# Kernel optimization log

Hardware: AMD Instinct MI355X
Metric: run time of the kernel (lower is better)

The kernel has to match this reference:

```python
import jax, jax.numpy as jnp
import numpy as np

T, B, C, H, W = 128, 16, 4, 84, 84
NUM_ACTIONS, FEAT, HID = 18, 512, 256


def _conv(x, w, b, stride):
    # x: (N,C,H,W), w: (O,I,kh,kw)
    y = jax.lax.conv_general_dilated(
        x, w, window_strides=(stride, stride), padding='VALID',
        dimension_numbers=('NCHW', 'OIHW', 'NCHW'))
    return y + b[None, :, None, None]


def setup_inputs() -> dict:
    key = jax.random.key(0)
    ks = jax.random.split(key, 24)
    s = 0.05
    inp = {
        'obs_seq': jax.random.uniform(ks[0], (T, B, C, H, W), jnp.float32) * 255.0,
        'actions_seq': jax.random.randint(ks[1], (T, B), 0, NUM_ACTIONS),
        'episode_starts_seq': jax.random.randint(ks[2], (T, B), 0, 2).astype(jnp.float32),
        'h0': jnp.zeros((1, B, HID), jnp.float32),
        'c0': jnp.zeros((1, B, HID), jnp.float32),
        # NatureCNN params
        'conv1_w': jax.random.normal(ks[3], (32, C, 8, 8)) * s,
        'conv1_b': jnp.zeros((32,)),
        'conv2_w': jax.random.normal(ks[4], (64, 32, 4, 4)) * s,
        'conv2_b': jnp.zeros((64,)),
        'conv3_w': jax.random.normal(ks[5], (64, 64, 3, 3)) * s,
        'conv3_b': jnp.zeros((64,)),
        'fc_w': jax.random.normal(ks[6], (FEAT, 64 * 7 * 7)) * s,
        'fc_b': jnp.zeros((FEAT,)),
        # LSTM params (torch gate order i,f,g,o)
        'w_ih': jax.random.normal(ks[7], (4 * HID, FEAT)) * s,
        'w_hh': jax.random.normal(ks[8], (4 * HID, HID)) * s,
        'b_ih': jnp.zeros((4 * HID,)),
        'b_hh': jnp.zeros((4 * HID,)),
        # heads
        'actor_w': jax.random.normal(ks[9], (NUM_ACTIONS, HID)) * 0.01,
        'actor_b': jnp.zeros((NUM_ACTIONS,)),
        'critic_w': jax.random.normal(ks[10], (1, HID)) * s,
        'critic_b': jnp.zeros((1,)),
        'aux_w': jax.random.normal(ks[11], (1, FEAT)) * s,
        'aux_b': jnp.zeros((1,)),
    }
    return inp


def reference(obs_seq, actions_seq, episode_starts_seq, h0, c0,
              conv1_w, conv1_b, conv2_w, conv2_b, conv3_w, conv3_b,
              fc_w, fc_b, w_ih, w_hh, b_ih, b_hh,
              actor_w, actor_b, critic_w, critic_b, aux_w, aux_b):
    t, b = actions_seq.shape
    x = obs_seq.reshape(t * b, *obs_seq.shape[2:]) / 255.0
    x = jax.nn.relu(_conv(x, conv1_w, conv1_b, 4))   # (TB,32,20,20)
    x = jax.nn.relu(_conv(x, conv2_w, conv2_b, 2))   # (TB,64,9,9)
    x = jax.nn.relu(_conv(x, conv3_w, conv3_b, 1))   # (TB,64,7,7)
    feat = jax.nn.relu(x.reshape(t * b, -1) @ fc_w.T + fc_b)  # (TB,FEAT)

    aux_logits = (feat @ aux_w.T + aux_b).squeeze(-1).reshape(t, b)
    feat_seq = feat.reshape(t, b, -1)

    def step(carry, inp):
        h, c = carry
        x_t, s_t = inp
        keep = (1.0 - s_t)[:, None]
        h = h * keep
        c = c * keep
        gates = x_t @ w_ih.T + b_ih + h @ w_hh.T + b_hh  # (B,4H)
        i, f, g, o = jnp.split(gates, 4, axis=-1)
        c = jax.nn.sigmoid(f) * c + jax.nn.sigmoid(i) * jnp.tanh(g)
        h = jax.nn.sigmoid(o) * jnp.tanh(c)
        return (h, c), h

    _, out = jax.lax.scan(step, (h0[0], c0[0]), (feat_seq, episode_starts_seq))  # (T,B,HID)

    logits = out @ actor_w.T + actor_b
    logp = jax.nn.log_softmax(logits, axis=-1)
    log_probs = jnp.take_along_axis(logp, actions_seq[..., None], axis=-1).squeeze(-1)
    entropy = -jnp.sum(jnp.exp(logp) * logp, axis=-1)
    values = (out @ critic_w.T + critic_b).squeeze(-1)
    return log_probs, entropy, values, aux_logits
```

## Files before the change

kernel.cpp:

```cpp
#include <hip/hip_runtime.h>
#include <hip/hip_bf16.h>
#include <cstddef>

typedef __attribute__((ext_vector_type(8))) short bf16x8;
typedef __attribute__((ext_vector_type(8))) unsigned short u16x8;
typedef __attribute__((ext_vector_type(4))) float f32x4;

static constexpr size_t OFF_X1B   = 0;
static constexpr size_t OFF_X2B   = 52428800;
static constexpr size_t OFF_X3B   = 73662464;
static constexpr size_t OFF_FEATB = 86507520;
static constexpr size_t OFF_W2B   = 88604672;
static constexpr size_t OFF_W3B   = 88670208;
static constexpr size_t OFF_FCWB  = 88743936;
static constexpr size_t OFF_WIHB  = 91955200;
static constexpr size_t OFF_GX    = 97198080;
static constexpr size_t OFF_HSEQ  = 105586688;
static constexpr size_t OFF_W1B   = 108732416;
static constexpr size_t OFF_WHHB  = 108748800;
static constexpr size_t OFF_ORDB  = 109273088;
static constexpr size_t OFF_ORDT0 = 109281280;
static constexpr size_t OFF_ORDLEN= 109289472;
static constexpr size_t OFF_NSEG  = 109297664;
static constexpr size_t OFF_FCPART= 109305856;

__device__ __forceinline__ float sigmoidf_(float x) {
  return 1.0f / (1.0f + __expf(-x));
}
__device__ __forceinline__ float tanhf_(float x) {
  return 1.0f - 2.0f / (__expf(2.0f * x) + 1.0f);
}
__device__ __forceinline__ unsigned short f2bfu(float x) {
  union { __hip_bfloat16 b; unsigned short u; } cv;
  cv.b = __float2bfloat16(x);
  return cv.u;
}

__global__ __launch_bounds__(256) void prep_kernel(
    const float* __restrict__ c1w, const float* __restrict__ c2w,
    const float* __restrict__ c3w, const float* __restrict__ fcw,
    const float* __restrict__ wih, const float* __restrict__ whh,
    __hip_bfloat16* __restrict__ w1b,
    __hip_bfloat16* __restrict__ w2b, __hip_bfloat16* __restrict__ w3b,
    __hip_bfloat16* __restrict__ fcwb, __hip_bfloat16* __restrict__ wihb,
    __hip_bfloat16* __restrict__ whhb) {
  int i = blockIdx.x * 256 + threadIdx.x;
  if (i < 32768) {
    int o = i >> 9, k = i & 511;
    int pos = k >> 5, ci = k & 31;
    int ky = pos >> 2, kx = pos & 3;
    w2b[i] = __float2bfloat16(c2w[o * 512 + ci * 16 + ky * 4 + kx]);
  } else if (i < 69632) {
    int j = i - 32768;
    int o = j / 576, k = j - o * 576;
    int pos = k >> 6, ci = k & 63;
    int ky = pos / 3, kx = pos - ky * 3;
    w3b[j] = __float2bfloat16(c3w[o * 576 + ci * 9 + ky * 3 + kx]);
  } else if (i < 1675264) {
    int j = i - 69632;
    int o = j / 3136, k = j - o * 3136;
    int sp = k >> 6, ci = k & 63;
    fcwb[j] = __float2bfloat16(fcw[o * 3136 + ci * 49 + sp]);
  } else if (i < 2199552) {
    int j = i - 1675264;
    wihb[j] = __float2bfloat16(wih[j]);
  } else if (i < 2461696) {
    int j = i - 2199552;
    whhb[j] = __float2bfloat16(whh[j]);
  } else if (i < 2469888) {
    int j = i - 2461696;
    int oc = j >> 8, k = j & 255;
    int ky = k >> 5, rem = k & 31;
    int ci = rem >> 3, kx = rem & 7;
    w1b[j] = __float2bfloat16(c1w[oc * 256 + ci * 64 + ky * 8 + kx] * (1.0f / 255.0f));
  }
}

__global__ __launch_bounds__(256) void plan_kernel(
    const float* __restrict__ starts, int* __restrict__ ord_b,
    int* __restrict__ ord_t0, int* __restrict__ ord_len,
    int* __restrict__ nseg_out) {
  __shared__ float s_starts[2048];
  __shared__ int s_t0[2048];
  __shared__ int s_len[2048];
  __shared__ int cnt[16];
  __shared__ int hist[132];
  __shared__ int off[132];
  const int tid = threadIdx.x;
  {
    float4* d = (float4*)s_starts;
    const float4* s = (const float4*)starts;
#pragma unroll
    for (int i = 0; i < 2; ++i) d[tid + i * 256] = s[tid + i * 256];
  }
  if (tid < 132) hist[tid] = 0;
  __syncthreads();
  if (tid < 16) {
    int b = tid, c = 0;
    for (int t = 0; t < 128; ++t) {
      float s = s_starts[t * 16 + b];
      if (t == 0 || s != 0.0f) {
        if (c > 0) s_len[b * 128 + c - 1] = t - s_t0[b * 128 + c - 1];
        s_t0[b * 128 + c] = t;
        ++c;
      }
    }
    s_len[b * 128 + c - 1] = 128 - s_t0[b * 128 + c - 1];
    cnt[b] = c;
  }
  __syncthreads();
  for (int idx = tid; idx < 2048; idx += 256) {
    int b = idx >> 7, i = idx & 127;
    if (i < cnt[b]) atomicAdd(&hist[s_len[idx]], 1);
  }
  __syncthreads();
  if (tid == 0) {
    int running = 0;
    for (int L = 128; L >= 1; --L) { off[L] = running; running += hist[L]; }
    *nseg_out = running;
  }
  __syncthreads();
  for (int idx = tid; idx < 2048; idx += 256) {
    int b = idx >> 7, i = idx & 127;
    if (i < cnt[b]) {
      int len = s_len[idx];
      int pos = atomicAdd(&off[len], 1);
      ord_b[pos] = b;
      ord_t0[pos] = s_t0[idx];
      ord_len[pos] = len;
    }
  }
}

__global__ __launch_bounds__(256, 2) void conv1_img(
    const float* __restrict__ obs, const __hip_bfloat16* __restrict__ w1b,
    const float* __restrict__ bias1, __hip_bfloat16* __restrict__ x1b) {
  constexpr int LDW = 264;
  __shared__ __align__(16) __hip_bfloat16 img[28224];
  __shared__ __align__(16) __hip_bfloat16 Ws[32 * LDW];
  const int tid = threadIdx.x;
  const int wv = tid >> 6, l = tid & 63;
  const int lane16 = l & 15, quad = l >> 4;
  const int n = blockIdx.x;

  for (int i = tid; i < 1024; i += 256) {
    const int r = i >> 5, c = (i & 31) * 8;
    *(uint4*)&Ws[r * LDW + c] = *(const uint4*)&w1b[r * 256 + c];
  }
  const float4* obs4 = (const float4*)(obs + (size_t)n * 28224);
  for (int j = tid; j < 7056; j += 256) {
    const float4 v = obs4[j];
    const int xq = j % 21;
    const int yc = j / 21;
    const int c = yc / 84, y = yc - c * 84;
    ushort4 w;
    w.x = f2bfu(v.x); w.y = f2bfu(v.y); w.z = f2bfu(v.z); w.w = f2bfu(v.w);
    *(ushort4*)&img[(y * 4 + c) * 84 + xq * 4] = w;
  }
  __syncthreads();

  const float bb0 = bias1[lane16];
  const float bb1 = bias1[16 + lane16];
  const __hip_bfloat16* wr0 = &Ws[lane16 * LDW];
  const __hip_bfloat16* wr1 = &Ws[(16 + lane16) * LDW];

  for (int f = wv; f < 25; f += 4) {
    const int sp = f * 16 + lane16;
    const int oy = sp / 20, ox = sp - oy * 20;
    const int ab = ((oy * 4) * 4 + quad) * 84 + ox * 4;
    f32x4 acc0 = {}, acc1 = {};
#pragma unroll
    for (int s = 0; s < 8; ++s) {
      const int ib = ab + s * 4 * 84;
      const ushort4 lo = *(const ushort4*)&img[ib];
      const ushort4 hi = *(const ushort4*)&img[ib + 4];
      bf16x8 a;
      a[0] = (short)lo.x; a[1] = (short)lo.y; a[2] = (short)lo.z; a[3] = (short)lo.w;
      a[4] = (short)hi.x; a[5] = (short)hi.y; a[6] = (short)hi.z; a[7] = (short)hi.w;
      const bf16x8 b0 = *(const bf16x8*)&wr0[s * 32 + quad * 8];
      const bf16x8 b1v = *(const bf16x8*)&wr1[s * 32 + quad * 8];
      acc0 = __builtin_amdgcn_mfma_f32_16x16x32_bf16(a, b0, acc0, 0, 0, 0);
      acc1 = __builtin_amdgcn_mfma_f32_16x16x32_bf16(a, b1v, acc1, 0, 0, 0);
    }
#pragma unroll
    for (int r = 0; r < 4; ++r) {
      const size_t row = (size_t)n * 400 + f * 16 + quad * 4 + r;
      x1b[row * 32 + lane16] = __float2bfloat16(fmaxf(acc0[r] + bb0, 0.f));
      x1b[row * 32 + 16 + lane16] = __float2bfloat16(fmaxf(acc1[r] + bb1, 0.f));
    }
  }
}

template<int KK, int LDW, int MODE>
__global__ __launch_bounds__(256, 2) void conv_rs(
    const __hip_bfloat16* __restrict__ A, const __hip_bfloat16* __restrict__ Wb,
    const float* __restrict__ bias, __hip_bfloat16* __restrict__ Cb) {
  __shared__ __align__(16) __hip_bfloat16 Ws[64 * LDW];
  const int tid = threadIdx.x;
  const int wv = tid >> 6, l = tid & 63;
  const int lane16 = l & 15, quad = l >> 4;
  constexpr int CPR = KK / 8;
  constexpr int CH = 64 * CPR;
  for (int i = tid; i < CH; i += 256) {
    const int r = i / CPR;
    const int c = (i - r * CPR) * 8;
    *(uint4*)&Ws[r * LDW + c] = *(const uint4*)&Wb[r * KK + c];
  }
  const int m0 = blockIdx.x * 256 + wv * 64;
  const __hip_bfloat16* abase[4];
#pragma unroll
  for (int mf = 0; mf < 4; ++mf) {
    const int m = m0 + mf * 16 + lane16;
    if (MODE == 1) {
      const int n = m / 81, sp = m - n * 81;
      const int oy = sp / 9, ox = sp - oy * 9;
      abase[mf] = A + ((n * 20 + oy * 2) * 20 + ox * 2) * 32 + quad * 8;
    } else {
      const int n = m / 49, sp = m - n * 49;
      const int oy = sp / 7, ox = sp - oy * 7;
      abase[mf] = A + ((n * 9 + oy) * 9 + ox) * 64 + quad * 8;
    }
  }
  f32x4 acc[4][4] = {};
  __syncthreads();
  constexpr int KS = KK / 32;
#pragma unroll
  for (int s = 0; s < KS; ++s) {
    int koff;
    if (MODE == 1) {
      koff = ((s >> 2) * 20 + (s & 3)) * 32;
    } else {
      const int pos = s >> 1;
      koff = ((pos / 3) * 9 + (pos % 3)) * 64 + (s & 1) * 32;
    }
    bf16x8 bfr[4];
#pragma unroll
    for (int nf = 0; nf < 4; ++nf)
      bfr[nf] = *(const bf16x8*)&Ws[(nf * 16 + lane16) * LDW + s * 32 + quad * 8];
#pragma unroll
    for (int mf = 0; mf < 4; ++mf) {
      const bf16x8 a = *(const bf16x8*)(abase[mf] + koff);
#pragma unroll
      for (int nf = 0; nf < 4; ++nf)
        acc[mf][nf] = __builtin_amdgcn_mfma_f32_16x16x32_bf16(a, bfr[nf], acc[mf][nf], 0, 0, 0);
    }
  }
#pragma unroll
  for (int nf = 0; nf < 4; ++nf) {
    const int col = nf * 16 + lane16;
    const float bb = bias[col];
#pragma unroll
    for (int mf = 0; mf < 4; ++mf)
#pragma unroll
      for (int r = 0; r < 4; ++r) {
        const int row = m0 + mf * 16 + quad * 4 + r;
        Cb[(size_t)row * 64 + col] =
            __float2bfloat16(fmaxf(acc[mf][nf][r] + bb, 0.f));
      }
  }
}

template<int BM, int MODE>
__global__ __launch_bounds__(256) void gemm_mfma(
    const __hip_bfloat16* __restrict__ Abase,
    const __hip_bfloat16* __restrict__ Wb,
    const float* __restrict__ bias1, const float* __restrict__ bias2,
    float* __restrict__ Cf, __hip_bfloat16* __restrict__ Cb,
    const int M, const int N, const int K, const int relu,
    float* __restrict__ Cpart) {
  constexpr int LDK = 40;
  __shared__ __align__(16) __hip_bfloat16 As[BM * LDK];
  __shared__ __align__(16) __hip_bfloat16 Ws[64 * LDK];
  const int tid = threadIdx.x;
  const int m0 = blockIdx.y * BM;
  const int n0 = blockIdx.x * 64;
  const int l = tid & 63;
  const int wv = tid >> 6;
  const int lane16 = l & 15;
  const int quad = l >> 4;
  constexpr int NF = (BM == 128) ? 4 : 2;
  const int m_base = (BM == 128) ? wv * 32 : (wv & 1) * 32;
  const int n_base = (BM == 128) ? 0 : (wv >> 1) * 32;
  constexpr int NCA = (BM == 128) ? 2 : 1;

  f32x4 acc[2][NF] = {};

  const __hip_bfloat16* arow[NCA];
  int acp[NCA];
#pragma unroll
  for (int c = 0; c < NCA; ++c) {
    const int id = tid + c * 256;
    const int row = id >> 2, cpos = id & 3;
    const int m = m0 + row;
    acp[c] = cpos;
    arow[c] = Abase + (size_t)m * K + cpos * 8;
  }
  const int wrow = tid >> 2, wcp = tid & 3;
  const __hip_bfloat16* wsrc = Wb + (size_t)(n0 + wrow) * K + wcp * 8;

  int s0 = 0, s1 = K >> 5;
  if (Cpart) {
    const int total = K >> 5;
    const int zz = blockIdx.z;
    const int q = total >> 2, rr = total & 3;
    s0 = zz * q + (zz < rr ? zz : rr);
    s1 = s0 + q + (zz < rr ? 1 : 0);
  }
  for (int s = s0; s < s1; ++s) {
    uint4 av[NCA];
#pragma unroll
    for (int c = 0; c < NCA; ++c) {
      av[c] = *(const uint4*)(arow[c] + s * 32);
    }
    const uint4 wval = *(const uint4*)(wsrc + s * 32);
    __syncthreads();
#pragma unroll
    for (int c = 0; c < NCA; ++c) {
      const int row = (tid + c * 256) >> 2;
      *(uint4*)&As[row * LDK + acp[c] * 8] = av[c];
    }
    *(uint4*)&Ws[wrow * LDK + wcp * 8] = wval;
    __syncthreads();
    const bf16x8 a0 = *(const bf16x8*)&As[(m_base + lane16) * LDK + quad * 8];
    const bf16x8 a1 = *(const bf16x8*)&As[(m_base + 16 + lane16) * LDK + quad * 8];
#pragma unroll
    for (int nf = 0; nf < NF; ++nf) {
      const bf16x8 b = *(const bf16x8*)&Ws[(n_base + nf * 16 + lane16) * LDK + quad * 8];
      acc[0][nf] = __builtin_amdgcn_mfma_f32_16x16x32_bf16(a0, b, acc[0][nf], 0, 0, 0);
      acc[1][nf] = __builtin_amdgcn_mfma_f32_16x16x32_bf16(a1, b, acc[1][nf], 0, 0, 0);
    }
  }
  if (Cpart) {
    float* dst = Cpart + (size_t)blockIdx.z * M * N;
#pragma unroll
    for (int nf = 0; nf < NF; ++nf) {
      const int col = n0 + n_base + nf * 16 + lane16;
#pragma unroll
      for (int mf = 0; mf < 2; ++mf) {
#pragma unroll
        for (int r = 0; r < 4; ++r) {
          const int row = m0 + m_base + mf * 16 + quad * 4 + r;
          dst[(size_t)row * N + col] = acc[mf][nf][r];
        }
      }
    }
    return;
  }
#pragma unroll
  for (int nf = 0; nf < NF; ++nf) {
    const int col = n0 + n_base + nf * 16 + lane16;
    float bb = bias1[col];
    if (bias2) bb += bias2[col];
#pragma unroll
    for (int mf = 0; mf < 2; ++mf) {
#pragma unroll
      for (int r = 0; r < 4; ++r) {
        const int row = m0 + m_base + mf * 16 + quad * 4 + r;
        float v = acc[mf][nf][r] + bb;
        if (relu) v = fmaxf(v, 0.f);
        if (Cf) Cf[(size_t)row * N + col] = v;
        if (Cb) Cb[(size_t)row * N + col] = __float2bfloat16(v);
      }
    }
  }
}

__global__ __launch_bounds__(256) void fc_reduce(
    const float* __restrict__ part, const float* __restrict__ fcb,
    const float* __restrict__ aux_w, const float* __restrict__ aux_b,
    __hip_bfloat16* __restrict__ featb, float* __restrict__ outp) {
  const int row = blockIdx.x;
  const int tid = threadIdx.x;
  __shared__ float red[256];
  float auxacc = 0.f;
#pragma unroll
  for (int h = 0; h < 2; ++h) {
    const int c = tid + h * 256;
    const size_t base = (size_t)row * 512 + c;
    float v = part[base] + part[1048576 + base] + part[2097152 + base] +
              part[3145728 + base];
    v += fcb[c];
    v = fmaxf(v, 0.f);
    featb[base] = __float2bfloat16(v);
    auxacc += v * aux_w[c];
  }
  red[tid] = auxacc;
  __syncthreads();
  for (int s = 128; s > 0; s >>= 1) {
    if (tid < s) red[tid] += red[tid + s];
    __syncthreads();
  }
  if (tid == 0) outp[6144 + row] = red[0] + aux_b[0];
}

__global__ __launch_bounds__(1024, 4) void lstm_mfma(
    const float* __restrict__ gx, const __hip_bfloat16* __restrict__ whhb,
    const float* __restrict__ starts, const float* __restrict__ h0,
    const float* __restrict__ c0, const int* __restrict__ ord_b,
    const int* __restrict__ ord_t0, const int* __restrict__ ord_len,
    const int* __restrict__ nseg_p, float* __restrict__ hseq) {
  constexpr int LDH = 264;
  constexpr int PS  = 1028;
  __shared__ __align__(16) __hip_bfloat16 h_lds[16 * LDH];
  __shared__ __align__(16) float pre[16 * PS];
  __shared__ int sg_b[16], sg_t0[16], sg_len[16];
  const int g = blockIdx.x;
  const int nseg = *nseg_p;
  if (g * 16 >= nseg) return;
  const int tid = threadIdx.x;
  const int wv = tid >> 6;
  const int l = tid & 63;
  const int lane16 = l & 15, quad = l >> 4;
  if (tid < 16) {
    const int s = g * 16 + tid;
    sg_b[tid] = (s < nseg) ? ord_b[s] : 0;
    sg_t0[tid] = (s < nseg) ? ord_t0[s] : 0;
    sg_len[tid] = (s < nseg) ? ord_len[s] : 0;
  }
  __syncthreads();
  bf16x8 bfrag[2][8];
#pragma unroll
  for (int nt = 0; nt < 2; ++nt)
#pragma unroll
    for (int ks = 0; ks < 8; ++ks)
      bfrag[nt][ks] = *(const bf16x8*)&whhb[
          (size_t)(wv * 64 + nt * 16 + lane16) * 256 + ks * 32 + quad * 8];
  const __hip_bfloat16* bs2 = &whhb[(size_t)(wv * 64 + 32 + lane16) * 256 + quad * 8];
  const __hip_bfloat16* bs3 = &whhb[(size_t)(wv * 64 + 48 + lane16) * 256 + quad * 8];

  const int m_own = wv;
  const int u = l * 4;
  const int b_own = sg_b[m_own];
  const int t0_own = sg_t0[m_own];
  const int len_own = sg_len[m_own];
  float4 c_reg = make_float4(0.f, 0.f, 0.f, 0.f);
  {
    float4 hv = make_float4(0.f, 0.f, 0.f, 0.f);
    if (len_own > 0 && t0_own == 0) {
      const float keep = 1.0f - starts[b_own];
      const float4 h4 = *(const float4*)&h0[b_own * 256 + u];
      const float4 c4 = *(const float4*)&c0[b_own * 256 + u];
      hv = make_float4(h4.x * keep, h4.y * keep, h4.z * keep, h4.w * keep);
      c_reg = make_float4(c4.x * keep, c4.y * keep, c4.z * keep, c4.w * keep);
    }
    __hip_bfloat16* hd = &h_lds[m_own * LDH + u];
    hd[0] = __float2bfloat16(hv.x); hd[1] = __float2bfloat16(hv.y);
    hd[2] = __float2bfloat16(hv.z); hd[3] = __float2bfloat16(hv.w);
  }
  const int maxlen = sg_len[0];
  for (int tt = 0; tt < maxlen; ++tt) {
    __syncthreads();
    f32x4 acc[4] = {};
#pragma unroll
    for (int ks = 0; ks < 8; ++ks) {
      const bf16x8 b2 = *(const bf16x8*)(bs2 + ks * 32);
      const bf16x8 b3 = *(const bf16x8*)(bs3 + ks * 32);
      const bf16x8 a = *(const bf16x8*)&h_lds[lane16 * LDH + ks * 32 + quad * 8];
      acc[0] = __builtin_amdgcn_mfma_f32_16x16x32_bf16(a, bfrag[0][ks], acc[0], 0, 0, 0);
      acc[1] = __builtin_amdgcn_mfma_f32_16x16x32_bf16(a, bfrag[1][ks], acc[1], 0, 0, 0);
      acc[2] = __builtin_amdgcn_mfma_f32_16x16x32_bf16(a, b2, acc[2], 0, 0, 0);
      acc[3] = __builtin_amdgcn_mfma_f32_16x16x32_bf16(a, b3, acc[3], 0, 0, 0);
    }
#pragma unroll
    for (int nt = 0; nt < 4; ++nt)
#pragma unroll
      for (int r = 0; r < 4; ++r)
        pre[(quad * 4 + r) * PS + wv * 64 + nt * 16 + lane16] = acc[nt][r];
    __syncthreads();
    if (tt < len_own) {
      const int t = t0_own + tt;
      const size_t gbase = (size_t)(t * 16 + b_own) * 1024 + u;
      const float4 g0 = *(const float4*)&gx[gbase];
      const float4 g1 = *(const float4*)&gx[gbase + 256];
      const float4 g2 = *(const float4*)&gx[gbase + 512];
      const float4 g3 = *(const float4*)&gx[gbase + 768];
      const float4 p0 = *(const float4*)&pre[m_own * PS + u];
      const float4 p1 = *(const float4*)&pre[m_own * PS + u + 256];
      const float4 p2 = *(const float4*)&pre[m_own * PS + u + 512];
      const float4 p3 = *(const float4*)&pre[m_own * PS + u + 768];
      const float i0 = sigmoidf_(p0.x + g0.x), i1 = sigmoidf_(p0.y + g0.y),
                  i2 = sigmoidf_(p0.z + g0.z), i3 = sigmoidf_(p0.w + g0.w);
      const float f0 = sigmoidf_(p1.x + g1.x), f1 = sigmoidf_(p1.y + g1.y),
                  f2 = sigmoidf_(p1.z + g1.z), f3 = sigmoidf_(p1.w + g1.w);
      const float q0 = tanhf_(p2.x + g2.x), q1 = tanhf_(p2.y + g2.y),
                  q2 = tanhf_(p2.z + g2.z), q3 = tanhf_(p2.w + g2.w);
      const float o0 = sigmoidf_(p3.x + g3.x), o1 = sigmoidf_(p3.y + g3.y),
                  o2 = sigmoidf_(p3.z + g3.z), o3 = sigmoidf_(p3.w + g3.w);
      c_reg.x = fmaf(f0, c_reg.x, i0 * q0);
      c_reg.y = fmaf(f1, c_reg.y, i1 * q1);
      c_reg.z = fmaf(f2, c_reg.z, i2 * q2);
      c_reg.w = fmaf(f3, c_reg.w, i3 * q3);
      const float4 h4 = make_float4(o0 * tanhf_(c_reg.x), o1 * tanhf_(c_reg.y),
                                    o2 * tanhf_(c_reg.z), o3 * tanhf_(c_reg.w));
      __hip_bfloat16* hd = &h_lds[m_own * LDH + u];
      hd[0] = __float2bfloat16(h4.x); hd[1] = __float2bfloat16(h4.y);
      hd[2] = __float2bfloat16(h4.z); hd[3] = __float2bfloat16(h4.w);
      *(float4*)&hseq[(size_t)(t * 16 + b_own) * 256 + u] = h4;
    }
  }
}

__global__ __launch_bounds__(256) void heads_kernel(
    const float* __restrict__ hseq, const int* __restrict__ actions,
    const float* __restrict__ actor_w, const float* __restrict__ actor_b,
    const float* __restrict__ critic_w, const float* __restrict__ critic_b,
    float* __restrict__ outp) {
  const int tid = threadIdx.x;
  const int wv = tid >> 6, l = tid & 63;
  const int tb = blockIdx.x * 4 + wv;
  const float4 h4 = *(const float4*)&hseq[(size_t)tb * 256 + l * 4];
  float part[19];
#pragma unroll
  for (int o = 0; o < 18; ++o) {
    const float4 w = *(const float4*)&actor_w[o * 256 + l * 4];
    part[o] = h4.x * w.x + h4.y * w.y + h4.z * w.z + h4.w * w.w;
  }
  {
    const float4 w = *(const float4*)&critic_w[l * 4];
    part[18] = h4.x * w.x + h4.y * w.y + h4.z * w.z + h4.w * w.w;
  }
#pragma unroll
  for (int off = 32; off > 0; off >>= 1) {
#pragma unroll
    for (int o = 0; o < 19; ++o) part[o] += __shfl_xor(part[o], off);
  }
  float lg[18];
  float m = -1e30f;
#pragma unroll
  for (int o = 0; o < 18; ++o) {
    lg[o] = part[o] + actor_b[o];
    m = fmaxf(m, lg[o]);
  }
  float se = 0.f;
#pragma unroll
  for (int o = 0; o < 18; ++o) se += __expf(lg[o] - m);
  const float lse = __logf(se);
  float ent = 0.f;
#pragma unroll
  for (int o = 0; o < 18; ++o) {
    const float lp = lg[o] - m - lse;
    ent -= __expf(lp) * lp;
  }
  if (l == 0) {
    const int a = actions[tb];
    outp[tb] = lg[a] - m - lse;
    outp[2048 + tb] = ent;
    outp[4096 + tb] = part[18] + critic_b[0];
  }
}

extern "C" void kernel_launch(void* const* d_in, const int* in_sizes, int n_in,
                              void* d_out, int out_size, void* d_ws, size_t ws_size,
                              hipStream_t stream) {
  const float* obs     = (const float*)d_in[0];
  const int*   actions = (const int*)d_in[1];
  const float* starts  = (const float*)d_in[2];
  const float* h0      = (const float*)d_in[3];
  const float* c0      = (const float*)d_in[4];
  const float* c1w     = (const float*)d_in[5];
  const float* c1b     = (const float*)d_in[6];
  const float* c2w     = (const float*)d_in[7];
  const float* c2b     = (const float*)d_in[8];
  const float* c3w     = (const float*)d_in[9];
  const float* c3b     = (const float*)d_in[10];
  const float* fcw     = (const float*)d_in[11];
  const float* fcb     = (const float*)d_in[12];
  const float* wih     = (const float*)d_in[13];
  const float* whh     = (const float*)d_in[14];
  const float* bih     = (const float*)d_in[15];
  const float* bhh     = (const float*)d_in[16];
  const float* aw      = (const float*)d_in[17];
  const float* ab      = (const float*)d_in[18];
  const float* cw      = (const float*)d_in[19];
  const float* cb      = (const float*)d_in[20];
  const float* auxw    = (const float*)d_in[21];
  const float* auxb    = (const float*)d_in[22];

  char* ws = (char*)d_ws;
  __hip_bfloat16* x1b   = (__hip_bfloat16*)(ws + OFF_X1B);
  __hip_bfloat16* x2b   = (__hip_bfloat16*)(ws + OFF_X2B);
  __hip_bfloat16* x3b   = (__hip_bfloat16*)(ws + OFF_X3B);
  __hip_bfloat16* featb = (__hip_bfloat16*)(ws + OFF_FEATB);
  __hip_bfloat16* w2b   = (__hip_bfloat16*)(ws + OFF_W2B);
  __hip_bfloat16* w3b   = (__hip_bfloat16*)(ws + OFF_W3B);
  __hip_bfloat16* fcwb  = (__hip_bfloat16*)(ws + OFF_FCWB);
  __hip_bfloat16* wihb  = (__hip_bfloat16*)(ws + OFF_WIHB);
  __hip_bfloat16* w1b   = (__hip_bfloat16*)(ws + OFF_W1B);
  __hip_bfloat16* whhb  = (__hip_bfloat16*)(ws + OFF_WHHB);
  float* gx   = (float*)(ws + OFF_GX);
  float* hseq = (float*)(ws + OFF_HSEQ);
  int* ord_b   = (int*)(ws + OFF_ORDB);
  int* ord_t0  = (int*)(ws + OFF_ORDT0);
  int* ord_len = (int*)(ws + OFF_ORDLEN);
  int* nseg    = (int*)(ws + OFF_NSEG);
  float* fcpart= (float*)(ws + OFF_FCPART);
  float* outp = (float*)d_out;

  prep_kernel<<<9648, 256, 0, stream>>>(c1w, c2w, c3w, fcw, wih, whh,
                                        w1b, w2b, w3b, fcwb, wihb, whhb);
  plan_kernel<<<1, 256, 0, stream>>>(starts, ord_b, ord_t0, ord_len, nseg);
  conv1_img<<<2048, 256, 0, stream>>>(obs, w1b, c1b, x1b);
  conv_rs<512, 520, 1><<<648, 256, 0, stream>>>(x1b, w2b, c2b, x2b);
  conv_rs<576, 584, 2><<<392, 256, 0, stream>>>(x2b, w3b, c3b, x3b);
  gemm_mfma<64, 0><<<dim3(8, 32, 4), 256, 0, stream>>>(
      x3b, fcwb, fcb, nullptr, nullptr, nullptr, 2048, 512, 3136, 0, fcpart);
  fc_reduce<<<2048, 256, 0, stream>>>(fcpart, fcb, auxw, auxb, featb, outp);
  gemm_mfma<64, 0><<<dim3(16, 32), 256, 0, stream>>>(
      featb, wihb, bih, bhh, gx, nullptr, 2048, 1024, 512, 0, nullptr);
  lstm_mfma<<<128, 1024, 0, stream>>>(gx, whhb, starts, h0, c0,
                                      ord_b, ord_t0, ord_len, nseg, hseq);
  heads_kernel<<<512, 256, 0, stream>>>(hseq, actions, aw, ab, cw, cb, outp);
}
```

Measured before the change: 658.3 us.

## Restructure conv stages with direct global-to-LDS loads and per-image blocks

```diff
diff --git a/kernel.cpp b/kernel.cpp
--- a/kernel.cpp
+++ b/kernel.cpp
@@ -3,26 +3,25 @@
 #include <cstddef>
 
 typedef __attribute__((ext_vector_type(8))) short bf16x8;
-typedef __attribute__((ext_vector_type(8))) unsigned short u16x8;
 typedef __attribute__((ext_vector_type(4))) float f32x4;
 
 static constexpr size_t OFF_X1B   = 0;
-static constexpr size_t OFF_X2B   = 52428800;
-static constexpr size_t OFF_X3B   = 73662464;
-static constexpr size_t OFF_FEATB = 86507520;
-static constexpr size_t OFF_W2B   = 88604672;
-static constexpr size_t OFF_W3B   = 88670208;
-static constexpr size_t OFF_FCWB  = 88743936;
-static constexpr size_t OFF_WIHB  = 91955200;
-static constexpr size_t OFF_GX    = 97198080;
-static constexpr size_t OFF_HSEQ  = 105586688;
-static constexpr size_t OFF_W1B   = 108732416;
-static constexpr size_t OFF_WHHB  = 108748800;
-static constexpr size_t OFF_ORDB  = 109273088;
-static constexpr size_t OFF_ORDT0 = 109281280;
-static constexpr size_t OFF_ORDLEN= 109289472;
-static constexpr size_t OFF_NSEG  = 109297664;
-static constexpr size_t OFF_FCPART= 109305856;
+static constexpr size_t OFF_X2B   = 65536000;
+static constexpr size_t OFF_X3B   = 89423872;
+static constexpr size_t OFF_FEATB = 102268928;
+static constexpr size_t OFF_W2B   = 104366080;
+static constexpr size_t OFF_W3B   = 104431616;
+static constexpr size_t OFF_FCWB  = 104505344;
+static constexpr size_t OFF_WIHB  = 107716608;
+static constexpr size_t OFF_GX    = 108765184;
+static constexpr size_t OFF_HSEQ  = 117153792;
+static constexpr size_t OFF_W1B   = 119250944;
+static constexpr size_t OFF_WHHB  = 119267328;
+static constexpr size_t OFF_ORDB  = 119791616;
+static constexpr size_t OFF_ORDT0 = 119799808;
+static constexpr size_t OFF_ORDLEN= 119808000;
+static constexpr size_t OFF_NSEG  = 119816192;
+static constexpr size_t OFF_FCPART= 119824384;
 
 __device__ __forceinline__ float sigmoidf_(float x) {
   return 1.0f / (1.0f + __expf(-x));
@@ -30,10 +29,15 @@
 __device__ __forceinline__ float tanhf_(float x) {
   return 1.0f - 2.0f / (__expf(2.0f * x) + 1.0f);
 }
-__device__ __forceinline__ unsigned short f2bfu(float x) {
-  union { __hip_bfloat16 b; unsigned short u; } cv;
+__device__ __forceinline__ short f2bfs(float x) {
+  union { __hip_bfloat16 b; short s; } cv;
   cv.b = __float2bfloat16(x);
-  return cv.u;
+  return cv.s;
+}
+__device__ __forceinline__ void dma16(const void* g, void* l) {
+  __builtin_amdgcn_global_load_lds(
+      (const __attribute__((address_space(1))) unsigned int*)g,
+      (__attribute__((address_space(3))) unsigned int*)l, 16, 0, 0);
 }
 
 __global__ __launch_bounds__(256) void prep_kernel(
@@ -132,131 +136,174 @@
   }
 }
 
-__global__ __launch_bounds__(256, 2) void conv1_img(
+__global__ __launch_bounds__(256, 2) void conv1_dma(
     const float* __restrict__ obs, const __hip_bfloat16* __restrict__ w1b,
     const float* __restrict__ bias1, __hip_bfloat16* __restrict__ x1b) {
   constexpr int LDW = 264;
-  __shared__ __align__(16) __hip_bfloat16 img[28224];
+  __shared__ __align__(16) float imgf[15552];
   __shared__ __align__(16) __hip_bfloat16 Ws[32 * LDW];
   const int tid = threadIdx.x;
   const int wv = tid >> 6, l = tid & 63;
   const int lane16 = l & 15, quad = l >> 4;
-  const int n = blockIdx.x;
+  const int n = blockIdx.x >> 1, h = blockIdx.x & 1;
 
   for (int i = tid; i < 1024; i += 256) {
     const int r = i >> 5, c = (i & 31) * 8;
     *(uint4*)&Ws[r * LDW + c] = *(const uint4*)&w1b[r * 256 + c];
   }
-  const float4* obs4 = (const float4*)(obs + (size_t)n * 28224);
-  for (int j = tid; j < 7056; j += 256) {
-    const float4 v = obs4[j];
-    const int xq = j % 21;
-    const int yc = j / 21;
-    const int c = yc / 84, y = yc - c * 84;
-    ushort4 w;
-    w.x = f2bfu(v.x); w.y = f2bfu(v.y); w.z = f2bfu(v.z); w.w = f2bfu(v.w);
-    *(ushort4*)&img[(y * 4 + c) * 84 + xq * 4] = w;
+  {
+    const char* gbase = (const char*)(obs + (size_t)n * 28224 + wv * 7056 + h * 3360);
+    char* lbase = (char*)imgf + wv * 15360;
+    for (int k = 0; k < 15; ++k) {
+      int off = k * 1024 + l * 16;
+      if (off >= 14784) off = 0;
+      dma16(gbase + off, lbase + k * 1024);
+    }
   }
   __syncthreads();
 
   const float bb0 = bias1[lane16];
   const float bb1 = bias1[16 + lane16];
-  const __hip_bfloat16* wr0 = &Ws[lane16 * LDW];
-  const __hip_bfloat16* wr1 = &Ws[(16 + lane16) * LDW];
-
-  for (int f = wv; f < 25; f += 4) {
+  for (int f = wv; f < 13; f += 4) {
     const int sp = f * 16 + lane16;
     const int oy = sp / 20, ox = sp - oy * 20;
-    const int ab = ((oy * 4) * 4 + quad) * 84 + ox * 4;
+    const float* ab = &imgf[quad * 3840 + (oy * 4) * 84 + ox * 4];
     f32x4 acc0 = {}, acc1 = {};
 #pragma unroll
     for (int s = 0; s < 8; ++s) {
-      const int ib = ab + s * 4 * 84;
-      const ushort4 lo = *(const ushort4*)&img[ib];
-      const ushort4 hi = *(const ushort4*)&img[ib + 4];
+      const f32x4 lo = *(const f32x4*)(ab + s * 84);
+      const f32x4 hi = *(const f32x4*)(ab + s * 84 + 4);
       bf16x8 a;
-      a[0] = (short)lo.x; a[1] = (short)lo.y; a[2] = (short)lo.z; a[3] = (short)lo.w;
-      a[4] = (short)hi.x; a[5] = (short)hi.y; a[6] = (short)hi.z; a[7] = (short)hi.w;
-      const bf16x8 b0 = *(const bf16x8*)&wr0[s * 32 + quad * 8];
-      const bf16x8 b1v = *(const bf16x8*)&wr1[s * 32 + quad * 8];
+      a[0] = f2bfs(lo[0]); a[1] = f2bfs(lo[1]); a[2] = f2bfs(lo[2]); a[3] = f2bfs(lo[3]);
+      a[4] = f2bfs(hi[0]); a[5] = f2bfs(hi[1]); a[6] = f2bfs(hi[2]); a[7] = f2bfs(hi[3]);
+      const bf16x8 b0 = *(const bf16x8*)&Ws[lane16 * LDW + s * 32 + quad * 8];
+      const bf16x8 b1 = *(const bf16x8*)&Ws[(16 + lane16) * LDW + s * 32 + quad * 8];
       acc0 = __builtin_amdgcn_mfma_f32_16x16x32_bf16(a, b0, acc0, 0, 0, 0);
-      acc1 = __builtin_amdgcn_mfma_f32_16x16x32_bf16(a, b1v, acc1, 0, 0, 0);
-    }
+      acc1 = __builtin_amdgcn_mfma_f32_16x16x32_bf16(a, b1, acc1, 0, 0, 0);
+    }
+    const size_t base = (size_t)n * 16000 + (size_t)(h * 200) * 40;
 #pragma unroll
     for (int r = 0; r < 4; ++r) {
-      const size_t row = (size_t)n * 400 + f * 16 + quad * 4 + r;
-      x1b[row * 32 + lane16] = __float2bfloat16(fmaxf(acc0[r] + bb0, 0.f));
-      x1b[row * 32 + 16 + lane16] = __float2bfloat16(fmaxf(acc1[r] + bb1, 0.f));
-    }
-  }
-}
-
-template<int KK, int LDW, int MODE>
-__global__ __launch_bounds__(256, 2) void conv_rs(
-    const __hip_bfloat16* __restrict__ A, const __hip_bfloat16* __restrict__ Wb,
-    const float* __restrict__ bias, __hip_bfloat16* __restrict__ Cb) {
-  __shared__ __align__(16) __hip_bfloat16 Ws[64 * LDW];
+      const int ml = f * 16 + quad * 4 + r;
+      if (ml < 200) {
+        x1b[base + ml * 40 + lane16] = __float2bfloat16(fmaxf(acc0[r] + bb0, 0.f));
+        x1b[base + ml * 40 + 16 + lane16] = __float2bfloat16(fmaxf(acc1[r] + bb1, 0.f));
+      }
+    }
+  }
+}
+
+__global__ __launch_bounds__(256, 2) void conv2_dma(
+    const __hip_bfloat16* __restrict__ x1b, const __hip_bfloat16* __restrict__ w2b,
+    const float* __restrict__ bias, __hip_bfloat16* __restrict__ x2b) {
+  constexpr int LDW = 520;
+  __shared__ __align__(16) __hip_bfloat16 img[24 * 800];
+  __shared__ __align__(16) __hip_bfloat16 Ws[32 * LDW];
   const int tid = threadIdx.x;
   const int wv = tid >> 6, l = tid & 63;
   const int lane16 = l & 15, quad = l >> 4;
-  constexpr int CPR = KK / 8;
-  constexpr int CH = 64 * CPR;
-  for (int i = tid; i < CH; i += 256) {
-    const int r = i / CPR;
-    const int c = (i - r * CPR) * 8;
-    *(uint4*)&Ws[r * LDW + c] = *(const uint4*)&Wb[r * KK + c];
-  }
-  const int m0 = blockIdx.x * 256 + wv * 64;
-  const __hip_bfloat16* abase[4];
-#pragma unroll
-  for (int mf = 0; mf < 4; ++mf) {
-    const int m = m0 + mf * 16 + lane16;
-    if (MODE == 1) {
-      const int n = m / 81, sp = m - n * 81;
-      const int oy = sp / 9, ox = sp - oy * 9;
-      abase[mf] = A + ((n * 20 + oy * 2) * 20 + ox * 2) * 32 + quad * 8;
-    } else {
-      const int n = m / 49, sp = m - n * 49;
-      const int oy = sp / 7, ox = sp - oy * 7;
-      abase[mf] = A + ((n * 9 + oy) * 9 + ox) * 64 + quad * 8;
-    }
-  }
-  f32x4 acc[4][4] = {};
-  __syncthreads();
-  constexpr int KS = KK / 32;
-#pragma unroll
-  for (int s = 0; s < KS; ++s) {
-    int koff;
-    if (MODE == 1) {
-      koff = ((s >> 2) * 20 + (s & 3)) * 32;
-    } else {
-      const int pos = s >> 1;
-      koff = ((pos / 3) * 9 + (pos % 3)) * 64 + (s & 1) * 32;
-    }
-    bf16x8 bfr[4];
-#pragma unroll
-    for (int nf = 0; nf < 4; ++nf)
-      bfr[nf] = *(const bf16x8*)&Ws[(nf * 16 + lane16) * LDW + s * 32 + quad * 8];
-#pragma unroll
-    for (int mf = 0; mf < 4; ++mf) {
-      const bf16x8 a = *(const bf16x8*)(abase[mf] + koff);
-#pragma unroll
-      for (int nf = 0; nf < 4; ++nf)
-        acc[mf][nf] = __builtin_amdgcn_mfma_f32_16x16x32_bf16(a, bfr[nf], acc[mf][nf], 0, 0, 0);
-    }
-  }
-#pragma unroll
-  for (int nf = 0; nf < 4; ++nf) {
-    const int col = nf * 16 + lane16;
-    const float bb = bias[col];
-#pragma unroll
-    for (int mf = 0; mf < 4; ++mf)
-#pragma unroll
-      for (int r = 0; r < 4; ++r) {
-        const int row = m0 + mf * 16 + quad * 4 + r;
-        Cb[(size_t)row * 64 + col] =
-            __float2bfloat16(fmaxf(acc[mf][nf][r] + bb, 0.f));
+  const int n = blockIdx.x >> 1, nh = blockIdx.x & 1;
+
+  for (int i = tid; i < 2048; i += 256) {
+    const int r = i >> 6, c = (i & 63) * 8;
+    *(uint4*)&Ws[r * LDW + c] = *(const uint4*)&w2b[(nh * 32 + r) * 512 + c];
+  }
+  {
+    const char* g = (const char*)(x1b + (size_t)n * 16000);
+    char* lb = (char*)img;
+    for (int i = 0; i < 8; ++i) {
+      const int k = wv * 8 + i;
+      int off = k * 1024 + l * 16;
+      if (off >= 32000) off = 0;
+      dma16(g + off, lb + k * 1024);
+    }
+  }
+  __syncthreads();
+
+  const int colg = nh * 32;
+  const float bb0 = bias[colg + lane16];
+  const float bb1 = bias[colg + 16 + lane16];
+  for (int f = wv; f < 6; f += 4) {
+    const int sp = f * 16 + lane16;
+    const int oy = sp / 9, ox = sp - oy * 9;
+    const __hip_bfloat16* ab = &img[((oy * 2) * 20 + ox * 2) * 40 + quad * 8];
+    f32x4 acc0 = {}, acc1 = {};
+#pragma unroll
+    for (int s = 0; s < 16; ++s) {
+      const int ky = s >> 2, kx = s & 3;
+      const bf16x8 a = *(const bf16x8*)(ab + (ky * 20 + kx) * 40);
+      const bf16x8 b0 = *(const bf16x8*)&Ws[lane16 * LDW + s * 32 + quad * 8];
+      const bf16x8 b1 = *(const bf16x8*)&Ws[(16 + lane16) * LDW + s * 32 + quad * 8];
+      acc0 = __builtin_amdgcn_mfma_f32_16x16x32_bf16(a, b0, acc0, 0, 0, 0);
+      acc1 = __builtin_amdgcn_mfma_f32_16x16x32_bf16(a, b1, acc1, 0, 0, 0);
+    }
+#pragma unroll
+    for (int r = 0; r < 4; ++r) {
+      const int ml = f * 16 + quad * 4 + r;
+      if (ml < 81) {
+        const size_t o = (size_t)n * 5832 + (size_t)ml * 72 + colg;
+        x2b[o + lane16] = __float2bfloat16(fmaxf(acc0[r] + bb0, 0.f));
+        x2b[o + 16 + lane16] = __float2bfloat16(fmaxf(acc1[r] + bb1, 0.f));
       }
+    }
+  }
+}
+
+__global__ __launch_bounds__(256, 3) void conv3_dma(
+    const __hip_bfloat16* __restrict__ x2b, const __hip_bfloat16* __restrict__ w3b,
+    const float* __restrict__ bias, __hip_bfloat16* __restrict__ x3b) {
+  constexpr int LDW = 584;
+  __shared__ __align__(16) __hip_bfloat16 img[12 * 648];
+  __shared__ __align__(16) __hip_bfloat16 Ws[32 * LDW];
+  const int tid = threadIdx.x;
+  const int wv = tid >> 6, l = tid & 63;
+  const int lane16 = l & 15, quad = l >> 4;
+  const int n = blockIdx.x >> 1, nh = blockIdx.x & 1;
+
+  for (int i = tid; i < 2304; i += 256) {
+    const int r = i / 72, c = (i - r * 72) * 8;
+    *(uint4*)&Ws[r * LDW + c] = *(const uint4*)&w3b[(nh * 32 + r) * 576 + c];
+  }
+  {
+    const char* g = (const char*)(x2b + (size_t)n * 5832);
+    char* lb = (char*)img;
+    for (int i = 0; i < 3; ++i) {
+      const int k = wv * 3 + i;
+      int off = k * 1024 + l * 16;
+      if (off >= 11664) off = 0;
+      dma16(g + off, lb + k * 1024);
+    }
+  }
+  __syncthreads();
+
+  const int colg = nh * 32;
+  const float bb0 = bias[colg + lane16];
+  const float bb1 = bias[colg + 16 + lane16];
+  {
+    const int f = wv;
+    const int sp = f * 16 + lane16;
+    const int oy = sp / 7, ox = sp - oy * 7;
+    const __hip_bfloat16* ab = &img[(oy * 9 + ox) * 72 + quad * 8];
+    f32x4 acc0 = {}, acc1 = {};
+#pragma unroll
+    for (int s = 0; s < 18; ++s) {
+      const int pos = s >> 1, half = s & 1;
+      const int ky = pos / 3, kx = pos - ky * 3;
+      const bf16x8 a = *(const bf16x8*)(ab + (ky * 9 + kx) * 72 + half * 32);
+      const bf16x8 b0 = *(const bf16x8*)&Ws[lane16 * LDW + s * 32 + quad * 8];
+      const bf16x8 b1 = *(const bf16x8*)&Ws[(16 + lane16) * LDW + s * 32 + quad * 8];
+      acc0 = __builtin_amdgcn_mfma_f32_16x16x32_bf16(a, b0, acc0, 0, 0, 0);
+      acc1 = __builtin_amdgcn_mfma_f32_16x16x32_bf16(a, b1, acc1, 0, 0, 0);
+    }
+#pragma unroll
+    for (int r = 0; r < 4; ++r) {
+      const int ml = f * 16 + quad * 4 + r;
+      if (ml < 49) {
+        const size_t o = (size_t)n * 3136 + (size_t)ml * 64 + colg;
+        x3b[o + lane16] = __float2bfloat16(fmaxf(acc0[r] + bb0, 0.f));
+        x3b[o + 16 + lane16] = __float2bfloat16(fmaxf(acc1[r] + bb1, 0.f));
+      }
+    }
   }
 }
 
@@ -599,9 +646,9 @@
   prep_kernel<<<9648, 256, 0, stream>>>(c1w, c2w, c3w, fcw, wih, whh,
                                         w1b, w2b, w3b, fcwb, wihb, whhb);
   plan_kernel<<<1, 256, 0, stream>>>(starts, ord_b, ord_t0, ord_len, nseg);
-  conv1_img<<<2048, 256, 0, stream>>>(obs, w1b, c1b, x1b);
-  conv_rs<512, 520, 1><<<648, 256, 0, stream>>>(x1b, w2b, c2b, x2b);
-  conv_rs<576, 584, 2><<<392, 256, 0, stream>>>(x2b, w3b, c3b, x3b);
+  conv1_dma<<<4096, 256, 0, stream>>>(obs, w1b, c1b, x1b);
+  conv2_dma<<<4096, 256, 0, stream>>>(x1b, w2b, c2b, x2b);
+  conv3_dma<<<4096, 256, 0, stream>>>(x2b, w3b, c3b, x3b);
   gemm_mfma<64, 0><<<dim3(8, 32, 4), 256, 0, stream>>>(
       x3b, fcwb, fcb, nullptr, nullptr, nullptr, 2048, 512, 3136, 0, fcpart);
   fc_reduce<<<2048, 256, 0, stream>>>(fcpart, fcb, auxw, auxb, featb, outp);
```

New measurement: 644.9 us. -2.0%, faster.
